# Performance work log

Hardware: AMD Instinct MI355X
Metric: run time of the kernel (lower is better)

Reference implementation:

```python
import jax, jax.numpy as jnp
import numpy as np

HMS_W, SCORE_W, OFF_W = 2.0, 1.0, 1.0   # Matcher init weights
GAMMA, BETA, ALPHA = 2.0, 4.0, 0.25     # focal-loss constants from source


def _single_cost(ph, ps, po, gh, go):
    """Cost matrix for one batch element.
    ph: [N,C,HW] logits, ps: [N,1] logits, po: [N,C,2] logits,
    gh: [n,C,HW] targets in [0,1], go: [n,C,2] targets. Returns [N,n].
    """
    mask_no_kp = gh.sum(-1) == 0                                   # [n,C]
    num_kp = jnp.clip((~mask_no_kp).sum(-1).astype(ph.dtype), 1.0)  # [n]

    # ---- heatmap focal cost (sigmoid_hms_cost) ----
    x = ph[:, None]                                                # [N,1,C,HW]
    t = gh[None]                                                   # [1,n,C,HW]
    # BCE-with-logits: softplus(x) - x*t (numerically stable)
    ce = jax.nn.softplus(x) - x * t                                # [N,n,C,HW]
    ce = jnp.where(mask_no_kp[None, :, :, None], 0.0, ce)
    p = jax.nn.sigmoid(x)
    eq1 = (gh == 1.0).astype(ph.dtype)[None]                       # [1,n,C,HW]
    p_t = ((1.0 - p) * eq1 + p * (1.0 - eq1)) ** GAMMA
    ratio = eq1 + ((1.0 - t) * (1.0 - eq1)) ** BETA
    hm_cost = (ce * p_t * ratio).sum((-1, -2)) / num_kp[None]      # [N,n]

    # ---- score focal cost (targets are all ones) ----
    sp = jax.nn.sigmoid(ps)                                        # [N,1]
    sc = ALPHA * jax.nn.softplus(-ps) * (1.0 - sp) ** GAMMA        # [N,1]
    score_cost = jnp.broadcast_to(sc, (ps.shape[0], gh.shape[0]))  # [N,n]

    # ---- offset L2 cost ----
    pred_off = jax.nn.sigmoid(po)[:, None]                         # [N,1,C,2]
    oc = ((pred_off - go[None]) ** 2).sum(-1)                      # [N,n,C]
    oc = jnp.where(mask_no_kp[None], 0.0, oc)
    off_cost = oc.sum(-1) / num_kp[None] / 2.0                     # [N,n]

    return HMS_W * hm_cost + SCORE_W * score_cost + OFF_W * off_cost


def setup_inputs() -> dict:
    key = jax.random.key(0)
    k1, k2, k3, k4, k5 = jax.random.split(key, 5)
    B, N, n, C, H, W = 2, 50, 15, 17, 64, 64
    return {
        "pred_hms": jax.random.normal(k1, (B, N, C, H, W), dtype=jnp.float32),
        "pred_scores": jax.random.normal(k2, (B, N, 1), dtype=jnp.float32),
        "pred_offsets": jax.random.normal(k3, (B, N, C, 2), dtype=jnp.float32),
        "gt_heatmaps": jax.random.uniform(k4, (B, n, C, H, W), dtype=jnp.float32),
        "gt_offsets": jax.random.uniform(k5, (B, n, C, 2), dtype=jnp.float32),
    }


def reference(pred_hms, pred_scores, pred_offsets, gt_heatmaps, gt_offsets):
    B, N, C, H, W = pred_hms.shape
    n = gt_heatmaps.shape[1]
    ph = pred_hms.reshape(B, N, C, H * W)
    gh = gt_heatmaps.reshape(B, n, C, H * W)
    # cost: [B, N, n] -- the Hungarian-matching cost matrices
    return jax.vmap(_single_cost)(ph, pred_scores, pred_offsets, gh, gt_offsets)
```

## Files before the change

### kernel.cpp

```cpp
#include <hip/hip_runtime.h>
#include <math.h>

#define B_  2
#define N_  50
#define n_  15
#define C_  17
#define HW_ 4096
#define KC  32
#define CHB 2176
#define PSTR 52
#define GSTR 20
#define REG_OFF 1024
#define RSZ 832
#define NOUT (B_*N_*n_)


__device__ __forceinline__ void pred_feats(float x, float& a1, float& a2, float& b1) {
    float e  = __expf(-fabsf(x));
    float L  = __logf(1.f + e);
    float r  = __builtin_amdgcn_rcpf(1.f + e);
    float p  = (x >= 0.f) ? r : e * r;
    float sp = fmaxf(x, 0.f) + L;
    float p2 = p * p;
    a1 = sp * p2;
    a2 = -x * p2;
    float om = 1.f - p;
    b1 = (sp - x) * om * om;
}

__global__ void mask_kernel(const float* __restrict__ gh, float* __restrict__ ws) {
    int c = blockIdx.x, j = blockIdx.y, b = blockIdx.z;
    const float* row = gh + (((size_t)(b * n_ + j)) * C_ + c) * HW_;
    int tid = threadIdx.x;
    int any = 0;
    for (int e = 0; e < 4; ++e) {
        float4 v = *(const float4*)(row + (size_t)e * 1024 + tid * 4);
        any |= (v.x != 0.f) | (v.y != 0.f) | (v.z != 0.f) | (v.w != 0.f);
    }
    __shared__ int s_any;
    if (tid == 0) s_any = 0;
    __syncthreads();
    if (any) atomicOr(&s_any, 1);
    __syncthreads();
    if (tid == 0) ws[(b * n_ + j) * C_ + c] = s_any ? 1.f : 0.f;
}

__global__ void numkp_kernel(float* __restrict__ ws) {
    int t = threadIdx.x;
    if (t < B_ * n_) {
        float cnt = 0.f;
        for (int c = 0; c < C_; ++c) cnt += ws[t * C_ + c];
        ws[512 + t] = fmaxf(cnt, 1.f);
    }
}

__global__ void scoreoff_kernel(const float* __restrict__ ps, const float* __restrict__ po,
                                const float* __restrict__ go, const float* __restrict__ ws,
                                float* __restrict__ out) {
    int idx = blockIdx.x * 256 + threadIdx.x;
    if (idx >= NOUT) return;
    int b = idx / (N_ * n_);
    int rem = idx % (N_ * n_);
    int i = rem / n_, j = rem % n_;

    float s  = ps[b * N_ + i];
    float e  = __expf(-fabsf(s));
    float L  = __logf(1.f + e);
    float spn = fmaxf(-s, 0.f) + L;
    float r  = __builtin_amdgcn_rcpf(1.f + e);
    float sig = (s >= 0.f) ? r : e * r;
    float om = 1.f - sig;
    float sc = 0.25f * spn * om * om;

    float off = 0.f;
    const float* nmrow = ws + (b * n_ + j) * C_;
    for (int c = 0; c < C_; ++c) {
        float nm = nmrow[c];
        if (nm != 0.f) {
            for (int d = 0; d < 2; ++d) {
                float x = po[((b * N_ + i) * C_ + c) * 2 + d];
                float g = go[((b * n_ + j) * C_ + c) * 2 + d];
                float ee = __expf(-fabsf(x));
                float rr = __builtin_amdgcn_rcpf(1.f + ee);
                float sg = (x >= 0.f) ? rr : ee * rr;
                float dd = sg - g;
                off += dd * dd;
            }
        }
    }
    out[idx] = sc + off / ws[512 + b * n_ + j] * 0.5f;
}

#define FMA4(acc, a, u) \
    acc.x = fmaf(a, u.x, acc.x); acc.y = fmaf(a, u.y, acc.y); \
    acc.z = fmaf(a, u.z, acc.z); acc.w = fmaf(a, u.w, acc.w);

__global__ __launch_bounds__(256) void hm_kernel(const float* __restrict__ ph,
                                                 const float* __restrict__ gh,
                                                 float* __restrict__ ws,
                                                 int cpb, int nreg) {
    __shared__ __align__(16) float smem[3 * KC * PSTR + 3 * KC * GSTR];
    float* sA1 = smem;
    float* sA2 = smem + KC * PSTR;
    float* sB1 = smem + 2 * KC * PSTR;
    float* sU  = smem + 3 * KC * PSTR;
    float* sV  = sU + KC * GSTR;
    float* sW  = sU + 2 * KC * GSTR;

    int rg = blockIdx.x, b = blockIdx.y;
    int tid = threadIdx.x;
    int w = tid >> 6, lane = tid & 63;
    int it = lane % 13, jt = lane / 13;
    bool active = lane < 52;
    int kk = tid & 31, slot = tid >> 5;

    float4 acc0 = make_float4(0.f, 0.f, 0.f, 0.f);
    float4 acc1 = acc0, acc2 = acc0, acc3 = acc0;

    for (int cc = 0; cc < cpb; ++cc) {
        int ci = rg * cpb + cc;
        int c  = ci >> 7;
        int k0 = (ci & 127) * KC;

        if (slot < 4) {
            float uq[4], vq[4], wq[4];
            for (int s = 0; s < 4; ++s) {
                int j = 4 * slot + s;
                float t = 0.f, scale = 0.f;
                if (j < n_) {
                    t = gh[(((size_t)(b * n_ + j)) * C_ + c) * HW_ + k0 + kk];
                    scale = ws[(b * n_ + j) * C_ + c] * 2.f / ws[512 + b * n_ + j];
                }
                float q = 1.f - t, u = q * q; u *= u;
                uq[s] = u * scale;
                vq[s] = t * u * scale;
                wq[s] = (t == 1.f) ? scale : 0.f;
            }
            *(float4*)&sU[kk * GSTR + 4 * slot] = make_float4(uq[0], uq[1], uq[2], uq[3]);
            *(float4*)&sV[kk * GSTR + 4 * slot] = make_float4(vq[0], vq[1], vq[2], vq[3]);
            *(float4*)&sW[kk * GSTR + 4 * slot] = make_float4(wq[0], wq[1], wq[2], wq[3]);
        }
        for (int q = slot; q < 13; q += 8) {
            float a1[4], a2[4], b1[4];
            for (int s = 0; s < 4; ++s) {
                int i = 4 * q + s;
                float x = (i < N_) ? ph[(((size_t)(b * N_ + i)) * C_ + c) * HW_ + k0 + kk] : 0.f;
                pred_feats(x, a1[s], a2[s], b1[s]);
            }
            *(float4*)&sA1[kk * PSTR + 4 * q] = make_float4(a1[0], a1[1], a1[2], a1[3]);
            *(float4*)&sA2[kk * PSTR + 4 * q] = make_float4(a2[0], a2[1], a2[2], a2[3]);
            *(float4*)&sB1[kk * PSTR + 4 * q] = make_float4(b1[0], b1[1], b1[2], b1[3]);
        }
        __syncthreads();

        if (active) {
#pragma unroll
            for (int k2 = 0; k2 < 8; ++k2) {
                int k = w * 8 + k2;
                float4 a1 = *(const float4*)&sA1[k * PSTR + 4 * it];
                float4 a2 = *(const float4*)&sA2[k * PSTR + 4 * it];
                float4 b1 = *(const float4*)&sB1[k * PSTR + 4 * it];
                float4 u4 = *(const float4*)&sU[k * GSTR + 4 * jt];
                float4 v4 = *(const float4*)&sV[k * GSTR + 4 * jt];
                float4 w4 = *(const float4*)&sW[k * GSTR + 4 * jt];
                FMA4(acc0, a1.x, u4) FMA4(acc0, a2.x, v4) FMA4(acc0, b1.x, w4)
                FMA4(acc1, a1.y, u4) FMA4(acc1, a2.y, v4) FMA4(acc1, b1.y, w4)
                FMA4(acc2, a1.z, u4) FMA4(acc2, a2.z, v4) FMA4(acc2, b1.z, w4)
                FMA4(acc3, a1.w, u4) FMA4(acc3, a2.w, v4) FMA4(acc3, b1.w, w4)
            }
        }
        __syncthreads();
    }

    float* scratch = smem;
    if (active) {
        float4 accs[4] = {acc0, acc1, acc2, acc3};
        for (int s = 0; s < 4; ++s)
            *(float4*)&scratch[w * RSZ + (4 * it + s) * 16 + 4 * jt] = accs[s];
    }
    __syncthreads();

    float* reg = ws + REG_OFF + ((size_t)(b * nreg + rg)) * RSZ;
    for (int v = tid; v < RSZ; v += 256) {
        float s = scratch[v] + scratch[RSZ + v] + scratch[2 * RSZ + v] + scratch[3 * RSZ + v];
        reg[v] = s;
    }
}

__global__ void reduce_kernel(const float* __restrict__ ws, float* __restrict__ out, int nreg) {
    int i = blockIdx.x, b = blockIdx.y;
    int j = threadIdx.x & 15, g = threadIdx.x >> 4;
    const float* base = ws + REG_OFF + ((size_t)b * nreg) * RSZ + i * 16 + j;
    float s = 0.f;
    for (int rg = g; rg < nreg; rg += 16)
        s += base[(size_t)rg * RSZ];
    __shared__ float red[16][17];
    red[g][j] = s;
    __syncthreads();
    if (g == 0 && j < n_) {
        float t = 0.f;
        for (int gg = 0; gg < 16; ++gg) t += red[gg][j];
        out[(b * N_ + i) * n_ + j] += t;
    }
}

extern "C" void kernel_launch(void* const* d_in, const int* in_sizes, int n_in,
                              void* d_out, int out_size, void* d_ws, size_t ws_size,
                              hipStream_t stream) {
    const float* ph = (const float*)d_in[0];
    const float* ps = (const float*)d_in[1];
    const float* po = (const float*)d_in[2];
    const float* gh = (const float*)d_in[3];
    const float* go = (const float*)d_in[4];
    float* out = (float*)d_out;
    float* ws  = (float*)d_ws;

    long availf = (long)(ws_size / 4);
    int cpb = 4;
    while (cpb < 128 && REG_OFF + 2L * (CHB / cpb) * RSZ > availf) cpb *= 2;
    int nreg = CHB / cpb;

    mask_kernel<<<dim3(C_, n_, B_), 256, 0, stream>>>(gh, ws);
    numkp_kernel<<<1, 64, 0, stream>>>(ws);
    scoreoff_kernel<<<(NOUT + 255) / 256, 256, 0, stream>>>(ps, po, go, ws, out);
    hm_kernel<<<dim3(nreg, B_), 256, 0, stream>>>(ph, gh, ws, cpb, nreg);
    reduce_kernel<<<dim3(N_, B_), 256, 0, stream>>>(ws, out, nreg);
}
```

Before: 132.0 us.

## Fold keypoint-mask detection into heatmap kernel and prefetch next chunk into registers

The separate mask and num-keypoint kernels, which reread the whole gt heatmap tensor, are removed. Nonzero-target detection now happens inside the heatmap kernel via per-block bitmask flags, and a small fold kernel turns those flags into masks and counts. Because the mask and normalisation are now applied per channel in the reduce kernel, hm_kernel no longer needs them up front. Global loads for the next chunk are also issued into registers before the current chunk's shared-memory compute, to overlap memory latency. This adds register pressure, a shared atomic, and a per-channel loop in the reduction.

Result: slower. 178.7 us (+35.4%).

```diff
diff --git a/kernel.cpp b/kernel.cpp
--- a/kernel.cpp
+++ b/kernel.cpp
@@ -10,10 +10,12 @@
 #define CHB 2176
 #define PSTR 52
 #define GSTR 20
-#define REG_OFF 1024
+#define MASK_OFF 0
+#define NKP_OFF 512
+#define FLAG_OFF 576
+#define REG_OFF 4096
 #define RSZ 832
 #define NOUT (B_*N_*n_)
-
 
 __device__ __forceinline__ void pred_feats(float x, float& a1, float& a2, float& b1) {
     float e  = __expf(-fabsf(x));
@@ -28,69 +30,6 @@
     b1 = (sp - x) * om * om;
 }
 
-__global__ void mask_kernel(const float* __restrict__ gh, float* __restrict__ ws) {
-    int c = blockIdx.x, j = blockIdx.y, b = blockIdx.z;
-    const float* row = gh + (((size_t)(b * n_ + j)) * C_ + c) * HW_;
-    int tid = threadIdx.x;
-    int any = 0;
-    for (int e = 0; e < 4; ++e) {
-        float4 v = *(const float4*)(row + (size_t)e * 1024 + tid * 4);
-        any |= (v.x != 0.f) | (v.y != 0.f) | (v.z != 0.f) | (v.w != 0.f);
-    }
-    __shared__ int s_any;
-    if (tid == 0) s_any = 0;
-    __syncthreads();
-    if (any) atomicOr(&s_any, 1);
-    __syncthreads();
-    if (tid == 0) ws[(b * n_ + j) * C_ + c] = s_any ? 1.f : 0.f;
-}
-
-__global__ void numkp_kernel(float* __restrict__ ws) {
-    int t = threadIdx.x;
-    if (t < B_ * n_) {
-        float cnt = 0.f;
-        for (int c = 0; c < C_; ++c) cnt += ws[t * C_ + c];
-        ws[512 + t] = fmaxf(cnt, 1.f);
-    }
-}
-
-__global__ void scoreoff_kernel(const float* __restrict__ ps, const float* __restrict__ po,
-                                const float* __restrict__ go, const float* __restrict__ ws,
-                                float* __restrict__ out) {
-    int idx = blockIdx.x * 256 + threadIdx.x;
-    if (idx >= NOUT) return;
-    int b = idx / (N_ * n_);
-    int rem = idx % (N_ * n_);
-    int i = rem / n_, j = rem % n_;
-
-    float s  = ps[b * N_ + i];
-    float e  = __expf(-fabsf(s));
-    float L  = __logf(1.f + e);
-    float spn = fmaxf(-s, 0.f) + L;
-    float r  = __builtin_amdgcn_rcpf(1.f + e);
-    float sig = (s >= 0.f) ? r : e * r;
-    float om = 1.f - sig;
-    float sc = 0.25f * spn * om * om;
-
-    float off = 0.f;
-    const float* nmrow = ws + (b * n_ + j) * C_;
-    for (int c = 0; c < C_; ++c) {
-        float nm = nmrow[c];
-        if (nm != 0.f) {
-            for (int d = 0; d < 2; ++d) {
-                float x = po[((b * N_ + i) * C_ + c) * 2 + d];
-                float g = go[((b * n_ + j) * C_ + c) * 2 + d];
-                float ee = __expf(-fabsf(x));
-                float rr = __builtin_amdgcn_rcpf(1.f + ee);
-                float sg = (x >= 0.f) ? rr : ee * rr;
-                float dd = sg - g;
-                off += dd * dd;
-            }
-        }
-    }
-    out[idx] = sc + off / ws[512 + b * n_ + j] * 0.5f;
-}
-
 #define FMA4(acc, a, u) \
     acc.x = fmaf(a, u.x, acc.x); acc.y = fmaf(a, u.y, acc.y); \
     acc.z = fmaf(a, u.z, acc.z); acc.w = fmaf(a, u.w, acc.w);
@@ -100,6 +39,7 @@
                                                  float* __restrict__ ws,
                                                  int cpb, int nreg) {
     __shared__ __align__(16) float smem[3 * KC * PSTR + 3 * KC * GSTR];
+    __shared__ unsigned s_flags;
     float* sA1 = smem;
     float* sA2 = smem + KC * PSTR;
     float* sB1 = smem + 2 * KC * PSTR;
@@ -114,43 +54,62 @@
     bool active = lane < 52;
     int kk = tid & 31, slot = tid >> 5;
 
-    float4 acc0 = make_float4(0.f, 0.f, 0.f, 0.f);
-    float4 acc1 = acc0, acc2 = acc0, acc3 = acc0;
-
-    for (int cc = 0; cc < cpb; ++cc) {
+    float rgt[4];
+    float rph[8];
+
+    auto issue = [&](int cc) {
         int ci = rg * cpb + cc;
         int c  = ci >> 7;
         int k0 = (ci & 127) * KC;
-
         if (slot < 4) {
+            for (int s = 0; s < 4; ++s) {
+                int j = 4 * slot + s;
+                rgt[s] = (j < n_) ? gh[(((size_t)(b * n_ + j)) * C_ + c) * HW_ + k0 + kk] : 0.f;
+            }
+        }
+        int qi = 0;
+        for (int q = slot; q < 13; q += 8, ++qi)
+            for (int s = 0; s < 4; ++s) {
+                int i = 4 * q + s;
+                rph[4 * qi + s] = (i < N_) ? ph[(((size_t)(b * N_ + i)) * C_ + c) * HW_ + k0 + kk] : 0.f;
+            }
+    };
+
+    issue(0);
+    if (tid == 0) s_flags = 0u;
+    __syncthreads();
+
+    float4 acc0 = make_float4(0.f, 0.f, 0.f, 0.f);
+    float4 acc1 = acc0, acc2 = acc0, acc3 = acc0;
+
+    for (int cc = 0; cc < cpb; ++cc) {
+        if (slot < 4) {
+            unsigned bits = 0;
             float uq[4], vq[4], wq[4];
             for (int s = 0; s < 4; ++s) {
-                int j = 4 * slot + s;
-                float t = 0.f, scale = 0.f;
-                if (j < n_) {
-                    t = gh[(((size_t)(b * n_ + j)) * C_ + c) * HW_ + k0 + kk];
-                    scale = ws[(b * n_ + j) * C_ + c] * 2.f / ws[512 + b * n_ + j];
-                }
-                float q = 1.f - t, u = q * q; u *= u;
-                uq[s] = u * scale;
-                vq[s] = t * u * scale;
-                wq[s] = (t == 1.f) ? scale : 0.f;
-            }
+                float t = rgt[s];
+                if (t != 0.f) bits |= 1u << (4 * slot + s);
+                float q1 = 1.f - t, u = q1 * q1; u *= u;
+                uq[s] = u;
+                vq[s] = t * u;
+                wq[s] = (t == 1.f) ? 1.f : 0.f;
+            }
+            if (bits) atomicOr(&s_flags, bits);
             *(float4*)&sU[kk * GSTR + 4 * slot] = make_float4(uq[0], uq[1], uq[2], uq[3]);
             *(float4*)&sV[kk * GSTR + 4 * slot] = make_float4(vq[0], vq[1], vq[2], vq[3]);
             *(float4*)&sW[kk * GSTR + 4 * slot] = make_float4(wq[0], wq[1], wq[2], wq[3]);
         }
-        for (int q = slot; q < 13; q += 8) {
-            float a1[4], a2[4], b1[4];
-            for (int s = 0; s < 4; ++s) {
-                int i = 4 * q + s;
-                float x = (i < N_) ? ph[(((size_t)(b * N_ + i)) * C_ + c) * HW_ + k0 + kk] : 0.f;
-                pred_feats(x, a1[s], a2[s], b1[s]);
-            }
-            *(float4*)&sA1[kk * PSTR + 4 * q] = make_float4(a1[0], a1[1], a1[2], a1[3]);
-            *(float4*)&sA2[kk * PSTR + 4 * q] = make_float4(a2[0], a2[1], a2[2], a2[3]);
-            *(float4*)&sB1[kk * PSTR + 4 * q] = make_float4(b1[0], b1[1], b1[2], b1[3]);
-        }
+        {
+            int qi = 0;
+            for (int q = slot; q < 13; q += 8, ++qi) {
+                float a1[4], a2[4], b1[4];
+                for (int s = 0; s < 4; ++s) pred_feats(rph[4 * qi + s], a1[s], a2[s], b1[s]);
+                *(float4*)&sA1[kk * PSTR + 4 * q] = make_float4(a1[0], a1[1], a1[2], a1[3]);
+                *(float4*)&sA2[kk * PSTR + 4 * q] = make_float4(a2[0], a2[1], a2[2], a2[3]);
+                *(float4*)&sB1[kk * PSTR + 4 * q] = make_float4(b1[0], b1[1], b1[2], b1[3]);
+            }
+        }
+        if (cc + 1 < cpb) issue(cc + 1);
         __syncthreads();
 
         if (active) {
@@ -179,28 +138,93 @@
             *(float4*)&scratch[w * RSZ + (4 * it + s) * 16 + 4 * jt] = accs[s];
     }
     __syncthreads();
-
     float* reg = ws + REG_OFF + ((size_t)(b * nreg + rg)) * RSZ;
-    for (int v = tid; v < RSZ; v += 256) {
-        float s = scratch[v] + scratch[RSZ + v] + scratch[2 * RSZ + v] + scratch[3 * RSZ + v];
-        reg[v] = s;
-    }
-}
-
-__global__ void reduce_kernel(const float* __restrict__ ws, float* __restrict__ out, int nreg) {
+    for (int v = tid; v < RSZ; v += 256)
+        reg[v] = scratch[v] + scratch[RSZ + v] + scratch[2 * RSZ + v] + scratch[3 * RSZ + v];
+    if (tid == 0) ((unsigned*)ws)[FLAG_OFF + b * nreg + rg] = s_flags;
+}
+
+__global__ void flagfold_kernel(float* __restrict__ ws, int nreg, int rpc) {
+    int t = threadIdx.x;
+    if (t >= B_ * n_) return;
+    int b = t / n_, j = t % n_;
+    const unsigned* flags = (const unsigned*)ws + FLAG_OFF + b * nreg;
+    float cnt = 0.f;
+    for (int c = 0; c < C_; ++c) {
+        unsigned any = 0;
+        for (int rr = 0; rr < rpc; ++rr) any |= flags[c * rpc + rr];
+        float m = ((any >> j) & 1u) ? 1.f : 0.f;
+        ws[MASK_OFF + (b * n_ + j) * C_ + c] = m;
+        cnt += m;
+    }
+    ws[NKP_OFF + b * n_ + j] = fmaxf(cnt, 1.f);
+}
+
+__global__ void scoreoff_kernel(const float* __restrict__ ps, const float* __restrict__ po,
+                                const float* __restrict__ go, const float* __restrict__ ws,
+                                float* __restrict__ out) {
+    int idx = blockIdx.x * 256 + threadIdx.x;
+    if (idx >= NOUT) return;
+    int b = idx / (N_ * n_);
+    int rem = idx % (N_ * n_);
+    int i = rem / n_, j = rem % n_;
+
+    float s  = ps[b * N_ + i];
+    float e  = __expf(-fabsf(s));
+    float L  = __logf(1.f + e);
+    float spn = fmaxf(-s, 0.f) + L;
+    float r  = __builtin_amdgcn_rcpf(1.f + e);
+    float sig = (s >= 0.f) ? r : e * r;
+    float om = 1.f - sig;
+    float sc = 0.25f * spn * om * om;
+
+    float off = 0.f;
+    const float* nmrow = ws + MASK_OFF + (b * n_ + j) * C_;
+    for (int c = 0; c < C_; ++c) {
+        float nm = nmrow[c];
+        if (nm != 0.f) {
+            for (int d = 0; d < 2; ++d) {
+                float x = po[((b * N_ + i) * C_ + c) * 2 + d];
+                float g = go[((b * n_ + j) * C_ + c) * 2 + d];
+                float ee = __expf(-fabsf(x));
+                float rr = __builtin_amdgcn_rcpf(1.f + ee);
+                float sg = (x >= 0.f) ? rr : ee * rr;
+                float dd = sg - g;
+                off += dd * dd;
+            }
+        }
+    }
+    out[idx] = sc + off / ws[NKP_OFF + b * n_ + j] * 0.5f;
+}
+
+__global__ void reduce_kernel(const float* __restrict__ ws, float* __restrict__ out,
+                              int nreg, int rpc) {
     int i = blockIdx.x, b = blockIdx.y;
-    int j = threadIdx.x & 15, g = threadIdx.x >> 4;
+    int t = threadIdx.x;
+    int j = t & 15, g = t >> 4;
+    __shared__ float sm[n_][C_];
+    __shared__ float sred[16][17];
+    if (t < n_ * C_) sm[t / C_][t % C_] = ws[MASK_OFF + (b * n_ + t / C_) * C_ + t % C_];
+    __syncthreads();
+
     const float* base = ws + REG_OFF + ((size_t)b * nreg) * RSZ + i * 16 + j;
+    bool ok = j < n_;
     float s = 0.f;
-    for (int rg = g; rg < nreg; rg += 16)
-        s += base[(size_t)rg * RSZ];
-    __shared__ float red[16][17];
-    red[g][j] = s;
-    __syncthreads();
-    if (g == 0 && j < n_) {
-        float t = 0.f;
-        for (int gg = 0; gg < 16; ++gg) t += red[gg][j];
-        out[(b * N_ + i) * n_ + j] += t;
+    for (int c = 0; c < C_; ++c) {
+        float m = ok ? sm[j][c] : 0.f;
+        if (m != 0.f) {
+            float ps = 0.f;
+            for (int rr = g; rr < rpc; rr += 16)
+                ps += base[(size_t)(c * rpc + rr) * RSZ];
+            s += m * ps;
+        }
+    }
+    sred[g][j] = s;
+    __syncthreads();
+    if (g == 0 && ok) {
+        float tt = 0.f;
+        for (int gg = 0; gg < 16; ++gg) tt += sred[gg][j];
+        out[(b * N_ + i) * n_ + j] += tt * 2.f / ws[NKP_OFF + b * n_ + j];
     }
 }
 
@@ -219,10 +243,10 @@
     int cpb = 4;
     while (cpb < 128 && REG_OFF + 2L * (CHB / cpb) * RSZ > availf) cpb *= 2;
     int nreg = CHB / cpb;
-
-    mask_kernel<<<dim3(C_, n_, B_), 256, 0, stream>>>(gh, ws);
-    numkp_kernel<<<1, 64, 0, stream>>>(ws);
+    int rpc  = 128 / cpb;
+
+    hm_kernel<<<dim3(nreg, B_), 256, 0, stream>>>(ph, gh, ws, cpb, nreg);
+    flagfold_kernel<<<1, 64, 0, stream>>>(ws, nreg, rpc);
     scoreoff_kernel<<<(NOUT + 255) / 256, 256, 0, stream>>>(ps, po, go, ws, out);
-    hm_kernel<<<dim3(nreg, B_), 256, 0, stream>>>(ph, gh, ws, cpb, nreg);
-    reduce_kernel<<<dim3(N_, B_), 256, 0, stream>>>(ws, out, nreg);
-}
+    reduce_kernel<<<dim3(N_, B_), 256, 0, stream>>>(ws, out, nreg, rpc);
+}
```
